# Kernel tuning notes

Hardware: AMD Instinct MI355X
Metric: run time of the kernel (lower is better)

## Reference

```python
import jax, jax.numpy as jnp
import numpy as np

N = 20000   # nodes
E = 320000  # edges (avg degree 16)
H = 4       # heads
C = 128     # per-head / output channels (concat=False -> mean over heads)
IN = 2      # init_channels (TSP coords)
NEG_SLOPE = 0.2


def setup_inputs() -> dict:
    key = jax.random.key(0)
    ks = jax.random.split(key, 32)
    s = 0.1
    def W(k, shape):
        return (jax.random.normal(k, shape, jnp.float32) * s)
    inp = {
        "x": jax.random.normal(ks[0], (N, IN), jnp.float32),
        "edge_index": jax.random.randint(ks[1], (2, E), 0, N, jnp.int32),
        "edge_attr": jax.random.uniform(ks[2], (E, 1), jnp.float32),
    }
    i = 3
    for b in range(2):  # two parallel GATBlocks
        inp[f"Wsrc{b}"]  = W(ks[i+0], (IN, H * C))
        inp[f"bsrc{b}"]  = jnp.zeros((H * C,), jnp.float32)
        inp[f"Wdst{b}"]  = W(ks[i+1], (IN, H * C))
        inp[f"bdst{b}"]  = jnp.zeros((H * C,), jnp.float32)
        inp[f"Wedge{b}"] = W(ks[i+2], (1, H * C))
        inp[f"att{b}"]   = W(ks[i+3], (H, C))
        inp[f"bias{b}"]  = jnp.zeros((C,), jnp.float32)
        inp[f"Wres{b}"]  = W(ks[i+4], (IN, C))  # SkipConnection projection (2 -> 128)
        i += 5
    inp["Wfuse"] = W(ks[i], (2 * C, C))
    inp["bfuse"] = jnp.zeros((C,), jnp.float32)
    return inp


def _gat_block(x, src, dst, ea, Wsrc, bsrc, Wdst, bdst, Wedge, att, bias, Wres):
    # GATv2Conv (concat=False) + ReLU + residual projection
    xs = (x @ Wsrc + bsrc).reshape(N, H, C)   # lin_l (source / message)
    xd = (x @ Wdst + bdst).reshape(N, H, C)   # lin_r (target)
    ee = (ea @ Wedge).reshape(-1, H, C)       # lin_edge
    e = jax.nn.leaky_relu(xs[src] + xd[dst] + ee, NEG_SLOPE)  # [Etot,H,C]
    logits = jnp.einsum('ehc,hc->eh', e, att)                 # [Etot,H]
    # segment softmax over incoming edges of each target node
    m = jax.ops.segment_max(logits, dst, num_segments=N)
    m = jnp.where(jnp.isfinite(m), m, 0.0)
    p = jnp.exp(logits - m[dst])
    denom = jax.ops.segment_sum(p, dst, num_segments=N)
    alpha = p / (denom[dst] + 1e-16)                          # [Etot,H]
    agg = jax.ops.segment_sum(xs[src] * alpha[:, :, None], dst, num_segments=N)
    out = agg.mean(axis=1) + bias                             # concat=False: mean heads
    return jax.nn.relu(out) + x @ Wres                        # ReLU then skip add


def reference(x, edge_index, edge_attr,
              Wsrc0, bsrc0, Wdst0, bdst0, Wedge0, att0, bias0, Wres0,
              Wsrc1, bsrc1, Wdst1, bdst1, Wedge1, att1, bias1, Wres1,
              Wfuse, bfuse):
    src, dst = edge_index[0], edge_index[1]
    # PyG default add_self_loops=True, fill_value='mean' for edge_attr
    loop = jnp.arange(N, dtype=src.dtype)
    src_a = jnp.concatenate([src, loop])
    dst_a = jnp.concatenate([dst, loop])
    mean_attr = jnp.mean(edge_attr, axis=0, keepdims=True)
    ea = jnp.concatenate([edge_attr, jnp.broadcast_to(mean_attr, (N, 1))], axis=0)

    h0 = _gat_block(x, src_a, dst_a, ea, Wsrc0, bsrc0, Wdst0, bdst0, Wedge0, att0, bias0, Wres0)
    h1 = _gat_block(x, src_a, dst_a, ea, Wsrc1, bsrc1, Wdst1, bdst1, Wedge1, att1, bias1, Wres1)
    xc = jnp.concatenate([h0, h1], axis=-1)       # [N, 2C]
    return jax.nn.relu(xc @ Wfuse + bfuse)        # [N, C]
```

## Files before the change

kernel.cpp:

```cpp
#include <hip/hip_runtime.h>

#define HH 4
#define CC 128
#define NPB 64

typedef __attribute__((ext_vector_type(8))) short short8v;
typedef __attribute__((ext_vector_type(4))) float f32x4;
typedef _Float16 v2h __attribute__((ext_vector_type(2)));

static inline size_t roundup256(size_t x) { return (x + 255) & ~(size_t)255; }

static __device__ __forceinline__ unsigned short f2bf(float f) {
    unsigned int u = __float_as_uint(f);
    unsigned int r = (u + 0x7FFFu + ((u >> 16) & 1u)) >> 16;
    return (unsigned short)r;
}
static __device__ __forceinline__ v2h bch(unsigned int u) {
    v2h r;
    __builtin_memcpy(&r, &u, 4);
    return r;
}
static __device__ __forceinline__ unsigned int pkh(float a, float b) {
    v2h h = {(_Float16)a, (_Float16)b};
    unsigned int u;
    __builtin_memcpy(&u, &h, 4);
    return u;
}
#if __has_builtin(__builtin_amdgcn_fdot2)
#define FDOT2(a, b, c) __builtin_amdgcn_fdot2((a), (b), (c), false)
#else
#define FDOT2(a, b, c) \
    fmaf((float)(a).x, (float)(b).x, fmaf((float)(a).y, (float)(b).y, (c)))
#endif

__global__ __launch_bounds__(256) void prep_kernel(
    const int* __restrict__ ei, const float* __restrict__ eattr,
    float* __restrict__ meansum, float* __restrict__ Lin, int* __restrict__ cnt,
    const float* __restrict__ Wsrc0, const float* __restrict__ bsrc0,
    const float* __restrict__ Wdst0, const float* __restrict__ bdst0,
    const float* __restrict__ Wedge0, const float* __restrict__ att0,
    const float* __restrict__ Wsrc1, const float* __restrict__ bsrc1,
    const float* __restrict__ Wdst1, const float* __restrict__ bdst1,
    const float* __restrict__ Wedge1, const float* __restrict__ att1,
    const float* __restrict__ Wfuse,
    uint4* __restrict__ pwD, unsigned short* __restrict__ pwB, int E)
{
    int tid = blockIdx.x * 256 + threadIdx.x;
    int lane = threadIdx.x & 63, wid = threadIdx.x >> 6;
    float s = 0.f;
    if (tid < E) {
        atomicAdd(&cnt[ei[E + tid]], 1);
        s = eattr[tid];
    }
    #pragma unroll
    for (int off = 32; off > 0; off >>= 1) s += __shfl_down(s, off, 64);
    __shared__ float wsum[4];
    if (lane == 0) wsum[wid] = s;
    __syncthreads();
    if (threadIdx.x == 0)
        atomicAdd(meansum, wsum[0] + wsum[1] + wsum[2] + wsum[3]);

    if (blockIdx.x < 4) {
        int b = tid >> 9;
        int hc = tid & 511;
        int c = hc & 127;
        int h = hc >> 7;
        int bh = b * 4 + h;
        const float* Ws = b ? Wsrc1 : Wsrc0;
        const float* bs = b ? bsrc1 : bsrc0;
        const float* Wd = b ? Wdst1 : Wdst0;
        const float* bd = b ? bdst1 : bdst0;
        const float* We = b ? Wedge1 : Wedge0;
        const float* at = b ? att1 : att0;
        float A = Ws[hc], B = Ws[512 + hc];
        float C = Wd[hc], D = Wd[512 + hc];
        float Ec = We[hc];
        float F = bs[hc] + bd[hc];
        float a = at[hc];
        pwD[bh * 128 + c] = make_uint4(pkh(A, B), pkh(C, D), pkh(Ec, F),
                                       __float_as_uint(0.4f * a));
        float sa = 0.6f * a;
        float vals[6] = {sa * A, sa * B, sa * C, sa * D, sa * Ec, sa * F};
        #pragma unroll
        for (int k = 0; k < 6; ++k) {
            float v = vals[k];
            #pragma unroll
            for (int off = 32; off > 0; off >>= 1) v += __shfl_down(v, off, 64);
            vals[k] = v;
        }
        __shared__ float Ls[4][6];
        if (lane == 0) {
            #pragma unroll
            for (int k = 0; k < 6; ++k) Ls[wid][k] = vals[k];
        }
        __syncthreads();
        if (threadIdx.x < 12) {
            int w2 = threadIdx.x / 6;
            int k = threadIdx.x % 6;
            int bhg = blockIdx.x * 2 + w2;
            Lin[bhg * 6 + k] = Ls[w2 * 2][k] + Ls[w2 * 2 + 1][k];
        }
    }

    if (blockIdx.x >= 4 && blockIdx.x < 20) {
        int t2 = tid - 1024;
        int ct = t2 >> 9;
        int kc = (t2 >> 6) & 7;
        int l  = t2 & 63;
        int c = ct * 16 + (l & 15);
        int kb = kc * 32 + (l >> 4) * 8;
        unsigned short v[8];
        #pragma unroll
        for (int j = 0; j < 8; ++j)
            v[j] = f2bf(Wfuse[(kb + j) * CC + c]);
        unsigned short* dst = pwB + (size_t)t2 * 8;
        #pragma unroll
        for (int j = 0; j < 8; ++j) dst[j] = v[j];
    }
}

__global__ __launch_bounds__(1024) void scan_kernel(const int* __restrict__ cnt,
                                                    int* __restrict__ rowptr,
                                                    int* __restrict__ cur, int N) {
    const int CH = 32;
    int t = threadIdx.x;
    int base = t * CH;
    int local[CH];
    int s = 0;
    #pragma unroll
    for (int i = 0; i < CH; ++i) {
        int idx = base + i;
        int v = (idx < N) ? cnt[idx] + 1 : 0;
        local[i] = s;
        s += v;
    }
    __shared__ int sums[1024];
    sums[t] = s;
    __syncthreads();
    for (int off = 1; off < 1024; off <<= 1) {
        int v = (t >= off) ? sums[t - off] : 0;
        __syncthreads();
        sums[t] += v;
        __syncthreads();
    }
    int excl = sums[t] - s;
    #pragma unroll
    for (int i = 0; i < CH; ++i) {
        int idx = base + i;
        if (idx < N) {
            int v = excl + local[i];
            rowptr[idx] = v;
            cur[idx] = v;
        }
    }
    if (t == 1023) rowptr[N] = excl + s;
}

__global__ __launch_bounds__(256) void scatter_kernel(
    const int* __restrict__ ei, const float* __restrict__ x,
    const float* __restrict__ eattr, const float* __restrict__ meansum,
    int* __restrict__ cur, uint4* __restrict__ eh4, int N, int E) {
    int e = blockIdx.x * 256 + threadIdx.x;
    int Etot = E + N;
    if (e >= Etot) return;
    int src, dst;
    float ea;
    if (e < E) { src = ei[e]; dst = ei[E + e]; ea = eattr[e]; }
    else       { src = e - E; dst = src; ea = meansum[0] / (float)E; }
    int pos = atomicAdd(&cur[dst], 1);
    const float2* x2 = (const float2*)x;
    float2 xs = x2[src];
    float2 xd = x2[dst];
    eh4[pos] = make_uint4(pkh(xs.x, xs.y), pkh(xd.x, xd.y), pkh(ea, 1.f),
                          (unsigned)src);
}

__global__ __launch_bounds__(256) void logits_kernel(
    const uint4* __restrict__ eh4,
    const float* __restrict__ Lin,
    const uint4* __restrict__ pwD,
    float* __restrict__ p8, int nchunks)
{
    int blk = blockIdx.x;
    int bhp = blk / nchunks;
    int chunk = blk - bhp * nchunks;
    int t = threadIdx.x;
    int iA = chunk * 512 + t;
    int iB = iA + 256;
    uint4 eA = eh4[iA], eB = eh4[iB];
    v2h xsA = bch(eA.x), xdA = bch(eA.y), eaA = bch(eA.z);
    v2h xsB = bch(eB.x), xdB = bch(eB.y), eaB = bch(eB.z);

    #pragma unroll
    for (int bi = 0; bi < 2; ++bi) {
        int bh = bhp * 2 + bi;
        const uint4* wp = pwD + bh * 128;
        float a0 = 0.f, a1 = 0.f;
        #pragma unroll 8
        for (int c = 0; c < 128; ++c) {
            uint4 w = wp[c];
            v2h AB = bch(w.x), CD = bch(w.y), EF = bch(w.z);
            float G = __uint_as_float(w.w);
            float uA = FDOT2(AB, xsA, FDOT2(CD, xdA, FDOT2(EF, eaA, 0.f)));
            float uB = FDOT2(AB, xsB, FDOT2(CD, xdB, FDOT2(EF, eaB, 0.f)));
            a0 = fmaf(G, __builtin_fabsf(uA), a0);
            a1 = fmaf(G, __builtin_fabsf(uB), a1);
        }
        const float* Lp = Lin + bh * 6;
        float l0 = Lp[0], l1 = Lp[1], l2 = Lp[2], l3 = Lp[3], l4 = Lp[4], l5 = Lp[5];
        float lgA = fmaf(l0, (float)xsA.x, fmaf(l1, (float)xsA.y,
                    fmaf(l2, (float)xdA.x, fmaf(l3, (float)xdA.y,
                    fmaf(l4, (float)eaA.x, l5))))) + a0;
        float lgB = fmaf(l0, (float)xsB.x, fmaf(l1, (float)xsB.y,
                    fmaf(l2, (float)xdB.x, fmaf(l3, (float)xdB.y,
                    fmaf(l4, (float)eaB.x, l5))))) + a1;
        p8[(size_t)iA * 8 + bh] = __expf(lgA);
        p8[(size_t)iB * 8 + bh] = __expf(lgB);
    }
}

__global__ __launch_bounds__(512) void node_kernel(
    const float* __restrict__ x,
    const int* __restrict__ rowptr,
    const uint4* __restrict__ eh4,
    const float* __restrict__ p8,
    const float* __restrict__ Wsrc0, const float* __restrict__ bsrc0,
    const float* __restrict__ bias0, const float* __restrict__ Wres0,
    const float* __restrict__ Wsrc1, const float* __restrict__ bsrc1,
    const float* __restrict__ bias1, const float* __restrict__ Wres1,
    const unsigned short* __restrict__ pwB, const float* __restrict__ bfuse,
    float* __restrict__ out, int N)
{
    __shared__ __align__(16) unsigned short hb[NPB][264];
    __shared__ __align__(16) float Sl[NPB][24];
    int t = threadIdx.x;
    int n0 = blockIdx.x * NPB;
    const float2* x2 = (const float2*)x;

    {
        int g = t >> 3, bh = t & 7;
        int n = n0 + g;
        if (n < N) {
            int beg = rowptr[n], end = rowptr[n + 1];
            float s0 = 0.f, s1 = 0.f, sb = 0.f;
            for (int i = beg; i < end; ++i) {
                float p = p8[(size_t)i * 8 + bh];
                unsigned srcu = eh4[i].w;
                float2 xs = x2[srcu];
                s0 = fmaf(p, xs.x, s0);
                s1 = fmaf(p, xs.y, s1);
                sb += p;
            }
            float rin = 1.f / (sb + 1e-16f);
            Sl[g][bh * 3 + 0] = s0 * rin;
            Sl[g][bh * 3 + 1] = s1 * rin;
            Sl[g][bh * 3 + 2] = sb * rin;
        }
    }
    __syncthreads();

    int c = t & (CC - 1);
    int quarter = t >> 7;

    float w00[HH], w01[HH], wb0[HH], w10[HH], w11[HH], wb1[HH];
    #pragma unroll
    for (int h = 0; h < HH; ++h) {
        w00[h] = Wsrc0[h * CC + c];
        w01[h] = Wsrc0[512 + h * CC + c];
        wb0[h] = bsrc0[h * CC + c];
        w10[h] = Wsrc1[h * CC + c];
        w11[h] = Wsrc1[512 + h * CC + c];
        wb1[h] = bsrc1[h * CC + c];
    }
    float bi0 = bias0[c], bi1 = bias1[c];
    float r00 = Wres0[c], r01 = Wres0[CC + c];
    float r10 = Wres1[c], r11 = Wres1[CC + c];

    for (int ni = quarter; ni < NPB; ni += 4) {
        int n = n0 + ni;
        if (n < N) {
            float x0 = x[2 * n], x1 = x[2 * n + 1];
            const float4* Sp4 = (const float4*)&Sl[ni][0];
            float4 q0 = Sp4[0], q1 = Sp4[1], q2 = Sp4[2];
            float4 q3 = Sp4[3], q4 = Sp4[4], q5 = Sp4[5];
            float h0v, h1v;
            {
                float s0[HH] = {q0.x, q0.w, q1.z, q2.y};
                float s1[HH] = {q0.y, q1.x, q1.w, q2.z};
                float sb[HH] = {q0.z, q1.y, q2.x, q2.w};
                float acc = 0.f;
                #pragma unroll
                for (int h = 0; h < HH; ++h)
                    acc += fmaf(w00[h], s0[h], fmaf(w01[h], s1[h], wb0[h] * sb[h]));
                float o = fmaxf(acc * 0.25f + bi0, 0.f);
                h0v = o + x0 * r00 + x1 * r01;
            }
            {
                float s0[HH] = {q3.x, q3.w, q4.z, q5.y};
                float s1[HH] = {q3.y, q4.x, q4.w, q5.z};
                float sb[HH] = {q3.z, q4.y, q5.x, q5.w};
                float acc = 0.f;
                #pragma unroll
                for (int h = 0; h < HH; ++h)
                    acc += fmaf(w10[h], s0[h], fmaf(w11[h], s1[h], wb1[h] * sb[h]));
                float o = fmaxf(acc * 0.25f + bi1, 0.f);
                h1v = o + x0 * r10 + x1 * r11;
            }
            hb[ni][c] = f2bf(h0v);
            hb[ni][CC + c] = f2bf(h1v);
        }
    }
    __syncthreads();

    int w = t >> 6;
    int l = t & 63;
    int nt = w & 3;
    int cthalf = w >> 2;
    int row = nt * 16 + (l & 15);

    short8v a[8];
    #pragma unroll
    for (int kc = 0; kc < 8; ++kc)
        a[kc] = *reinterpret_cast<const short8v*>(&hb[row][kc * 32 + (l >> 4) * 8]);

    const short8v* pB = reinterpret_cast<const short8v*>(pwB);
    #pragma unroll
    for (int ci = 0; ci < 4; ++ci) {
        int ct = cthalf * 4 + ci;
        f32x4 acc = {0.f, 0.f, 0.f, 0.f};
        #pragma unroll
        for (int kc = 0; kc < 8; ++kc) {
            short8v b = pB[(ct * 8 + kc) * 64 + l];
            acc = __builtin_amdgcn_mfma_f32_16x16x32_bf16(a[kc], b, acc, 0, 0, 0);
        }
        int ch = ct * 16 + (l & 15);
        float bi = bfuse[ch];
        #pragma unroll
        for (int j = 0; j < 4; ++j) {
            int n = n0 + nt * 16 + (l >> 4) * 4 + j;
            if (n < N) out[(size_t)n * CC + ch] = fmaxf(acc[j] + bi, 0.f);
        }
    }
}

extern "C" void kernel_launch(void* const* d_in, const int* in_sizes, int n_in,
                              void* d_out, int out_size, void* d_ws, size_t ws_size,
                              hipStream_t stream) {
    const float* x      = (const float*)d_in[0];
    const int*   ei     = (const int*)d_in[1];
    const float* eattr  = (const float*)d_in[2];
    const float* Wsrc0  = (const float*)d_in[3];
    const float* bsrc0  = (const float*)d_in[4];
    const float* Wdst0  = (const float*)d_in[5];
    const float* bdst0  = (const float*)d_in[6];
    const float* Wedge0 = (const float*)d_in[7];
    const float* att0   = (const float*)d_in[8];
    const float* bias0  = (const float*)d_in[9];
    const float* Wres0  = (const float*)d_in[10];
    const float* Wsrc1  = (const float*)d_in[11];
    const float* bsrc1  = (const float*)d_in[12];
    const float* Wdst1  = (const float*)d_in[13];
    const float* bdst1  = (const float*)d_in[14];
    const float* Wedge1 = (const float*)d_in[15];
    const float* att1   = (const float*)d_in[16];
    const float* bias1  = (const float*)d_in[17];
    const float* Wres1  = (const float*)d_in[18];
    const float* Wfuse  = (const float*)d_in[19];
    const float* bfuse  = (const float*)d_in[20];
    float* out = (float*)d_out;

    int N = in_sizes[0] / 2;
    int E = in_sizes[1] / 2;
    int Etot = E + N;
    int EtotPad = (Etot + 511) & ~511;

    size_t off = 0;
    float* meansum = (float*)((char*)d_ws + off);  off += 256;
    int*   cnt     = (int*)((char*)d_ws + off);    off += roundup256((size_t)N * sizeof(int));
    size_t zero_bytes = off;
    float* Lin     = (float*)((char*)d_ws + off);  off += 256;
    int*   cur     = (int*)((char*)d_ws + off);    off += roundup256((size_t)N * sizeof(int));
    int*   rowptr  = (int*)((char*)d_ws + off);    off += roundup256((size_t)(N + 1) * sizeof(int));
    uint4* pwD     = (uint4*)((char*)d_ws + off);  off += roundup256(1024 * sizeof(uint4));
    unsigned short* pwB = (unsigned short*)((char*)d_ws + off);
                                                   off += roundup256(4096 * 8 * sizeof(unsigned short));
    uint4* eh4     = (uint4*)((char*)d_ws + off);  off += roundup256((size_t)EtotPad * sizeof(uint4));
    float* p8      = (float*)((char*)d_ws + off);  off += roundup256((size_t)EtotPad * 8 * sizeof(float));

    hipMemsetAsync(d_ws, 0, zero_bytes, stream);

    prep_kernel<<<(E + 255) / 256, 256, 0, stream>>>(
        ei, eattr, meansum, Lin, cnt,
        Wsrc0, bsrc0, Wdst0, bdst0, Wedge0, att0,
        Wsrc1, bsrc1, Wdst1, bdst1, Wedge1, att1,
        Wfuse, pwD, pwB, E);

    scan_kernel<<<1, 1024, 0, stream>>>(cnt, rowptr, cur, N);

    scatter_kernel<<<(Etot + 255) / 256, 256, 0, stream>>>(
        ei, x, eattr, meansum, cur, eh4, N, E);

    int nchunks = EtotPad / 512;
    logits_kernel<<<4 * nchunks, 256, 0, stream>>>(
        eh4, Lin, pwD, p8, nchunks);

    node_kernel<<<(N + NPB - 1) / NPB, 512, 0, stream>>>(
        x, rowptr, eh4, p8,
        Wsrc0, bsrc0, bias0, Wres0,
        Wsrc1, bsrc1, bias1, Wres1,
        pwB, bfuse, out, N);
}
```

Baseline: 175.0 us.

## Restructure logits kernel: one wave per head-block, 4 edges per lane, coalesced stores

The logits kernel now assigns each of 8 waves in a 512-thread block to one (block, head) weight row and has every lane process 4 edges, so each weight load is reused across 4 edges instead of 2. The 8 exp-logits per edge are staged in shared memory and written out as coalesced float4 stores, replacing the previous strided 4-byte scattered writes. This cuts redundant edge-record loads (each edge is loaded once per block rather than once per head-pair block) at the cost of more registers per thread and a block-wide barrier.

```diff
diff --git a/kernel.cpp b/kernel.cpp
--- a/kernel.cpp
+++ b/kernel.cpp
@@ -3,6 +3,7 @@
 #define HH 4
 #define CC 128
 #define NPB 64
+#define LEB 256
 
 typedef __attribute__((ext_vector_type(8))) short short8v;
 typedef __attribute__((ext_vector_type(4))) float f32x4;
@@ -175,48 +176,57 @@
                           (unsigned)src);
 }
 
-__global__ __launch_bounds__(256) void logits_kernel(
+__global__ __launch_bounds__(512) void logits_kernel(
     const uint4* __restrict__ eh4,
     const float* __restrict__ Lin,
     const uint4* __restrict__ pwD,
-    float* __restrict__ p8, int nchunks)
+    float* __restrict__ p8)
 {
-    int blk = blockIdx.x;
-    int bhp = blk / nchunks;
-    int chunk = blk - bhp * nchunks;
+    __shared__ float plds[LEB][9];
     int t = threadIdx.x;
-    int iA = chunk * 512 + t;
-    int iB = iA + 256;
-    uint4 eA = eh4[iA], eB = eh4[iB];
-    v2h xsA = bch(eA.x), xdA = bch(eA.y), eaA = bch(eA.z);
-    v2h xsB = bch(eB.x), xdB = bch(eB.y), eaB = bch(eB.z);
-
-    #pragma unroll
-    for (int bi = 0; bi < 2; ++bi) {
-        int bh = bhp * 2 + bi;
-        const uint4* wp = pwD + bh * 128;
-        float a0 = 0.f, a1 = 0.f;
-        #pragma unroll 8
-        for (int c = 0; c < 128; ++c) {
-            uint4 w = wp[c];
-            v2h AB = bch(w.x), CD = bch(w.y), EF = bch(w.z);
-            float G = __uint_as_float(w.w);
-            float uA = FDOT2(AB, xsA, FDOT2(CD, xdA, FDOT2(EF, eaA, 0.f)));
-            float uB = FDOT2(AB, xsB, FDOT2(CD, xdB, FDOT2(EF, eaB, 0.f)));
-            a0 = fmaf(G, __builtin_fabsf(uA), a0);
-            a1 = fmaf(G, __builtin_fabsf(uB), a1);
-        }
-        const float* Lp = Lin + bh * 6;
-        float l0 = Lp[0], l1 = Lp[1], l2 = Lp[2], l3 = Lp[3], l4 = Lp[4], l5 = Lp[5];
-        float lgA = fmaf(l0, (float)xsA.x, fmaf(l1, (float)xsA.y,
-                    fmaf(l2, (float)xdA.x, fmaf(l3, (float)xdA.y,
-                    fmaf(l4, (float)eaA.x, l5))))) + a0;
-        float lgB = fmaf(l0, (float)xsB.x, fmaf(l1, (float)xsB.y,
-                    fmaf(l2, (float)xdB.x, fmaf(l3, (float)xdB.y,
-                    fmaf(l4, (float)eaB.x, l5))))) + a1;
-        p8[(size_t)iA * 8 + bh] = __expf(lgA);
-        p8[(size_t)iB * 8 + bh] = __expf(lgB);
-    }
+    int w = t >> 6, l = t & 63;
+    int base = blockIdx.x * LEB;
+
+    uint4 e[4];
+    #pragma unroll
+    for (int k = 0; k < 4; ++k) e[k] = eh4[base + k * 64 + l];
+    v2h xs[4], xd[4], ea[4];
+    #pragma unroll
+    for (int k = 0; k < 4; ++k) {
+        xs[k] = bch(e[k].x);
+        xd[k] = bch(e[k].y);
+        ea[k] = bch(e[k].z);
+    }
+
+    const uint4* wp = pwD + w * 128;
+    float acc[4] = {0.f, 0.f, 0.f, 0.f};
+    #pragma unroll 4
+    for (int c = 0; c < 128; ++c) {
+        uint4 wv = wp[c];
+        v2h AB = bch(wv.x), CD = bch(wv.y), EF = bch(wv.z);
+        float G = __uint_as_float(wv.w);
+        #pragma unroll
+        for (int k = 0; k < 4; ++k) {
+            float u = FDOT2(AB, xs[k], FDOT2(CD, xd[k], FDOT2(EF, ea[k], 0.f)));
+            acc[k] = fmaf(G, __builtin_fabsf(u), acc[k]);
+        }
+    }
+
+    const float* Lp = Lin + w * 6;
+    float l0 = Lp[0], l1 = Lp[1], l2 = Lp[2], l3 = Lp[3], l4 = Lp[4], l5 = Lp[5];
+    #pragma unroll
+    for (int k = 0; k < 4; ++k) {
+        float lg = fmaf(l0, (float)xs[k].x, fmaf(l1, (float)xs[k].y,
+                   fmaf(l2, (float)xd[k].x, fmaf(l3, (float)xd[k].y,
+                   fmaf(l4, (float)ea[k].x, l5))))) + acc[k];
+        plds[k * 64 + l][w] = __expf(lg);
+    }
+    __syncthreads();
+
+    int e2 = t >> 1, half = t & 1;
+    float4 v = make_float4(plds[e2][half * 4 + 0], plds[e2][half * 4 + 1],
+                           plds[e2][half * 4 + 2], plds[e2][half * 4 + 3]);
+    *(float4*)&p8[(size_t)(base + e2) * 8 + half * 4] = v;
 }
 
 __global__ __launch_bounds__(512) void node_kernel(
@@ -400,9 +410,7 @@
     scatter_kernel<<<(Etot + 255) / 256, 256, 0, stream>>>(
         ei, x, eattr, meansum, cur, eh4, N, E);
 
-    int nchunks = EtotPad / 512;
-    logits_kernel<<<4 * nchunks, 256, 0, stream>>>(
-        eh4, Lin, pwD, p8, nchunks);
+    logits_kernel<<<EtotPad / LEB, 512, 0, stream>>>(eh4, Lin, pwD, p8);
 
     node_kernel<<<(N + NPB - 1) / NPB, 512, 0, stream>>>(
         x, rowptr, eh4, p8,
```

Measured after the change: 181.0 us. 3.4% more time.
